# Kernel tuning notes

Hardware: AMD Instinct MI355X
Metric: run time of the kernel (lower is better)

## Reference

```python
import jax, jax.numpy as jnp
import numpy as np

NUM_EMBEDDINGS = 1024
EMBEDDING_DIM = 256
COMMITMENT_COST = 0.25


def setup_inputs() -> dict:
    key = jax.random.key(0)
    k_z, k_e = jax.random.split(key)
    z = jax.random.normal(k_z, (16, EMBEDDING_DIM, 4096), dtype=jnp.float32)
    # nn.Embedding init: uniform(-1/K, 1/K)
    emb = jax.random.uniform(
        k_e, (NUM_EMBEDDINGS, EMBEDDING_DIM), dtype=jnp.float32,
        minval=-1.0 / NUM_EMBEDDINGS, maxval=1.0 / NUM_EMBEDDINGS)
    return {"z": z, "emb": emb}


def reference(z, emb):
    # z: [B, D, T] -> [B, T, D]
    zt = jnp.transpose(z, (0, 2, 1))
    B, T, D = zt.shape
    flat = zt.reshape(-1, D)  # [N, D]
    dists = (jnp.sum(flat * flat, axis=1, keepdims=True)
             + jnp.sum(emb * emb, axis=1)
             - 2.0 * jnp.matmul(flat, emb.T))
    idx = jnp.argmin(dists, axis=1)          # [N]
    quantized = emb[idx].reshape(B, T, D)    # gather + reshape
    e_latent_loss = jnp.mean((jax.lax.stop_gradient(quantized) - zt) ** 2)
    q_latent_loss = jnp.mean((quantized - jax.lax.stop_gradient(zt)) ** 2)
    loss = q_latent_loss + COMMITMENT_COST * e_latent_loss
    # straight-through estimator
    quantized_st = zt + jax.lax.stop_gradient(quantized - zt)
    return jnp.transpose(quantized_st, (0, 2, 1)), loss
```

## Files before the change

kernel.cpp:

```cpp
#include <hip/hip_runtime.h>
#include <stdint.h>

#define B_   16
#define D_   256
#define T_   4096
#define K_   1024
#define N_   (B_ * T_)
#define BM   64

typedef __attribute__((ext_vector_type(4))) float floatx4;
typedef __attribute__((ext_vector_type(2))) float floatx2;
typedef __attribute__((ext_vector_type(2))) long longx2;

__global__ __launch_bounds__(256) void emb_prep(const float* __restrict__ emb,
                                                uint32_t* __restrict__ embf8,
                                                float* __restrict__ esqh,
                                                float* __restrict__ lossp) {
    int w = threadIdx.x >> 6, lane = threadIdx.x & 63;
    int k = blockIdx.x * 4 + w;
    float4 v = ((const float4*)emb)[k * 64 + lane];
    float a0 = v.x * 1024.f, a1 = v.y * 1024.f, a2 = v.z * 1024.f, a3 = v.w * 1024.f;
    int p = __builtin_amdgcn_cvt_pk_fp8_f32(a0, a1, 0, false);
    p = __builtin_amdgcn_cvt_pk_fp8_f32(a2, a3, p, true);
    int kk = lane >> 3, quad = (lane >> 1) & 3;
    int widx = (k >> 4) * 1024 + (kk >> 1) * 256 + (quad * 16 + (k & 15)) * 4
             + (kk & 1) * 2 + (lane & 1);
    embf8[widx] = (uint32_t)p;
    float ss = a0 * a0 + a1 * a1 + a2 * a2 + a3 * a3;
    #pragma unroll
    for (int off = 32; off; off >>= 1) ss += __shfl_xor(ss, off, 64);
    if (lane == 0) esqh[k] = ss * (0.5f / 1024.f);
    if (blockIdx.x == 0 && threadIdx.x == 0) *lossp = 0.f;
}

__global__ __launch_bounds__(256, 3) void vq_main(const float* __restrict__ z,
                                                  const uint32_t* __restrict__ embf8,
                                                  const float* __restrict__ esqh,
                                                  float* __restrict__ out0,
                                                  float* __restrict__ lossp) {
    __shared__ __align__(16) unsigned char xs[BM * 256];
    __shared__ float wvals[4][BM];
    __shared__ int   pidx[BM];
    __shared__ float zred[4];

    int tid  = threadIdx.x;
    int lane = tid & 63, w = tid >> 6;
    int ml   = lane & 15, quad = lane >> 4;
    int blk  = blockIdx.x;
    int b    = blk >> 6;
    int t0   = (blk & 63) * BM;
    const float* zb = z + (size_t)b * (D_ * T_) + t0;

    float zsq = 0.f;
    {
        int t = lane, hf = (t >> 4) & 1;
        #pragma unroll 2
        for (int j = 0; j < 8; ++j) {
            int dgrp = w + 4 * j;
            int d0 = dgrp * 8;
            float f0 = zb[(d0 + 0) * T_ + t];
            float f1 = zb[(d0 + 1) * T_ + t];
            float f2 = zb[(d0 + 2) * T_ + t];
            float f3 = zb[(d0 + 3) * T_ + t];
            float f4 = zb[(d0 + 4) * T_ + t];
            float f5 = zb[(d0 + 5) * T_ + t];
            float f6 = zb[(d0 + 6) * T_ + t];
            float f7 = zb[(d0 + 7) * T_ + t];
            zsq += f0*f0 + f1*f1 + f2*f2 + f3*f3 + f4*f4 + f5*f5 + f6*f6 + f7*f7;
            uint32_t p0 = (uint32_t)__builtin_amdgcn_cvt_pk_fp8_f32(f0, f1, 0, false);
            p0 = (uint32_t)__builtin_amdgcn_cvt_pk_fp8_f32(f2, f3, (int)p0, true);
            uint32_t p1 = (uint32_t)__builtin_amdgcn_cvt_pk_fp8_f32(f4, f5, 0, false);
            p1 = (uint32_t)__builtin_amdgcn_cvt_pk_fp8_f32(f6, f7, (int)p1, true);
            int c = dgrp >> 1, h = dgrp & 1;
            *(uint2*)&xs[t * 256 + ((c ^ (t & 15)) << 4) + ((h ^ hf) << 3)] =
                make_uint2(p0, p1);
        }
    }
    __syncthreads();

    long afr[4][8];
    #pragma unroll
    for (int s = 0; s < 4; ++s) {
        int pnt = s * 16 + ml;
        #pragma unroll
        for (int kk = 0; kk < 8; ++kk) {
            int c = 2 * kk + (quad >> 1), h = quad & 1;
            afr[s][kk] = *(const long*)&xs[pnt * 256 + ((c ^ ml) << 4) + ((h ^ (s & 1)) << 3)];
        }
    }

    float bv[4][4];
    #pragma unroll
    for (int s = 0; s < 4; ++s)
        #pragma unroll
        for (int i = 0; i < 4; ++i) bv[s][i] = 1e30f;

    int ct0 = w * 16;
    const char* ebL = (const char*)embf8 + (size_t)ct0 * 4096 + (size_t)lane * 16;
    const unsigned hi_mask = 0xFFFFFC00u;
    #pragma unroll 2
    for (int j = 0; j < 16; ++j) {
        const char* p = ebL + (size_t)j * 4096;
        longx2 qq[4];
        #pragma unroll
        for (int i = 0; i < 4; ++i)
            qq[i] = *(const longx2*)(p + i * 1024);
        float eh = esqh[(ct0 + j) * 16 + ml];
        floatx4 a0 = {0,0,0,0}, a1 = {0,0,0,0}, a2 = {0,0,0,0}, a3 = {0,0,0,0};
        #pragma unroll
        for (int i = 0; i < 4; ++i) {
            long bf0 = qq[i][0], bf1 = qq[i][1];
            a0 = __builtin_amdgcn_mfma_f32_16x16x32_fp8_fp8(afr[0][2*i],     bf0, a0, 0, 0, 0);
            a1 = __builtin_amdgcn_mfma_f32_16x16x32_fp8_fp8(afr[1][2*i],     bf0, a1, 0, 0, 0);
            a2 = __builtin_amdgcn_mfma_f32_16x16x32_fp8_fp8(afr[2][2*i],     bf0, a2, 0, 0, 0);
            a3 = __builtin_amdgcn_mfma_f32_16x16x32_fp8_fp8(afr[3][2*i],     bf0, a3, 0, 0, 0);
            a0 = __builtin_amdgcn_mfma_f32_16x16x32_fp8_fp8(afr[0][2*i + 1], bf1, a0, 0, 0, 0);
            a1 = __builtin_amdgcn_mfma_f32_16x16x32_fp8_fp8(afr[1][2*i + 1], bf1, a1, 0, 0, 0);
            a2 = __builtin_amdgcn_mfma_f32_16x16x32_fp8_fp8(afr[2][2*i + 1], bf1, a2, 0, 0, 0);
            a3 = __builtin_amdgcn_mfma_f32_16x16x32_fp8_fp8(afr[3][2*i + 1], bf1, a3, 0, 0, 0);
        }
        unsigned cbits = (unsigned)((ct0 + j) * 16 + ml);
        #pragma unroll
        for (int i = 0; i < 4; ++i) {
            float d0 = eh - a0[i];
            bv[0][i] = fminf(bv[0][i], __uint_as_float((__float_as_uint(d0) & hi_mask) | cbits));
            float d1 = eh - a1[i];
            bv[1][i] = fminf(bv[1][i], __uint_as_float((__float_as_uint(d1) & hi_mask) | cbits));
            float d2 = eh - a2[i];
            bv[2][i] = fminf(bv[2][i], __uint_as_float((__float_as_uint(d2) & hi_mask) | cbits));
            float d3 = eh - a3[i];
            bv[3][i] = fminf(bv[3][i], __uint_as_float((__float_as_uint(d3) & hi_mask) | cbits));
        }
    }

    #pragma unroll
    for (int s = 0; s < 4; ++s)
        #pragma unroll
        for (int i = 0; i < 4; ++i) {
            float v = bv[s][i];
            #pragma unroll
            for (int off = 1; off < 16; off <<= 1)
                v = fminf(v, __shfl_xor(v, off, 64));
            if (ml == 0) wvals[w][s * 16 + quad * 4 + i] = v;
        }
    #pragma unroll
    for (int off = 32; off; off >>= 1) zsq += __shfl_xor(zsq, off, 64);
    if (lane == 0) zred[w] = zsq;
    __syncthreads();

    if (tid < 64) {
        int t = tid;
        float wv = fminf(fminf(wvals[0][t], wvals[1][t]),
                         fminf(wvals[2][t], wvals[3][t]));
        pidx[t] = (int)(__float_as_uint(wv) & 1023u);
        float lsum = wv;
        #pragma unroll
        for (int off = 32; off; off >>= 1) lsum += __shfl_xor(lsum, off, 64);
        if (t == 0) {
            float tot = zred[0] + zred[1] + zred[2] + zred[3] + lsum * (2.0f / 1024.f);
            atomicAdd(lossp, tot * (1.25f / 16777216.0f));
        }
    }
    __syncthreads();

    #pragma unroll
    for (int m = 0; m < 4; ++m) {
        int t = (tid >> 4) + 16 * m;
        int g = tid & 15;
        int code = pidx[t];
        const char* src = (const char*)embf8 + (size_t)(code >> 4) * 4096
                        + (g >> 2) * 1024 + ((g & 3) * 16 + (code & 15)) * 16;
        uint4 v = *(const uint4*)src;
        *(uint4*)&xs[t * 256 + ((g ^ (t & 15)) << 4)] = v;
    }
    __syncthreads();

    float* ob = out0 + (size_t)b * (D_ * T_) + t0;
    {
        int t = lane;
        #pragma unroll
        for (int jj = 0; jj < 4; ++jj) {
            int g = w + 4 * jj;
            uint4 v = *(const uint4*)&xs[t * 256 + ((g ^ (t & 15)) << 4)];
            uint32_t wd[4] = {v.x, v.y, v.z, v.w};
            #pragma unroll
            for (int u = 0; u < 4; ++u) {
                int kk = (g >> 2) * 2 + (u >> 1);
                int d0 = kk * 32 + (g & 3) * 8 + (u & 1) * 4;
                floatx2 lo = __builtin_amdgcn_cvt_pk_f32_fp8((int)wd[u], false);
                floatx2 hi = __builtin_amdgcn_cvt_pk_f32_fp8((int)wd[u], true);
                ob[(d0 + 0) * T_ + t] = lo[0] * (1.f / 1024.f);
                ob[(d0 + 1) * T_ + t] = lo[1] * (1.f / 1024.f);
                ob[(d0 + 2) * T_ + t] = hi[0] * (1.f / 1024.f);
                ob[(d0 + 3) * T_ + t] = hi[1] * (1.f / 1024.f);
            }
        }
    }
}

extern "C" void kernel_launch(void* const* d_in, const int* in_sizes, int n_in,
                              void* d_out, int out_size, void* d_ws, size_t ws_size,
                              hipStream_t stream) {
    (void)in_sizes; (void)n_in; (void)out_size; (void)ws_size;
    const float* z   = (const float*)d_in[0];
    const float* emb = (const float*)d_in[1];

    uint32_t* embf8 = (uint32_t*)d_ws;
    float*    esqh  = (float*)((char*)d_ws + (size_t)K_ * D_);

    float* out0  = (float*)d_out;
    float* lossp = out0 + (size_t)N_ * D_;

    emb_prep<<<K_ / 4, 256, 0, stream>>>(emb, embf8, esqh, lossp);
    vq_main<<<N_ / BM, 256, 0, stream>>>(z, embf8, esqh, out0, lossp);
}
```

Before: 146.1 us.

## Halve point tile to 32 and split codebook across 8 waves per block

Reduces the points per block from 64 to 32 and uses 512 threads. Four waves cover the codebook quarters for each 16-point set, and each wave holds one set of A fragments and one accumulator. The goal is higher occupancy and fewer registers per wave. The cost is four times more codebook fragment loads per point and shorter contiguous z reads and output writes.

```diff
diff --git a/kernel.cpp b/kernel.cpp
--- a/kernel.cpp
+++ b/kernel.cpp
@@ -6,7 +6,7 @@
 #define T_   4096
 #define K_   1024
 #define N_   (B_ * T_)
-#define BM   64
+#define BM   32
 
 typedef __attribute__((ext_vector_type(4))) float floatx4;
 typedef __attribute__((ext_vector_type(2))) float floatx2;
@@ -33,30 +33,31 @@
     if (blockIdx.x == 0 && threadIdx.x == 0) *lossp = 0.f;
 }
 
-__global__ __launch_bounds__(256, 3) void vq_main(const float* __restrict__ z,
+__global__ __launch_bounds__(512, 8) void vq_main(const float* __restrict__ z,
                                                   const uint32_t* __restrict__ embf8,
                                                   const float* __restrict__ esqh,
                                                   float* __restrict__ out0,
                                                   float* __restrict__ lossp) {
     __shared__ __align__(16) unsigned char xs[BM * 256];
-    __shared__ float wvals[4][BM];
+    __shared__ float wvals[8][16];
     __shared__ int   pidx[BM];
-    __shared__ float zred[4];
+    __shared__ float zred[8];
 
     int tid  = threadIdx.x;
     int lane = tid & 63, w = tid >> 6;
     int ml   = lane & 15, quad = lane >> 4;
     int blk  = blockIdx.x;
-    int b    = blk >> 6;
-    int t0   = (blk & 63) * BM;
+    int b    = blk >> 7;
+    int t0   = (blk & 127) * BM;
     const float* zb = z + (size_t)b * (D_ * T_) + t0;
 
     float zsq = 0.f;
     {
-        int t = lane, hf = (t >> 4) & 1;
-        #pragma unroll 2
-        for (int j = 0; j < 8; ++j) {
-            int dgrp = w + 4 * j;
+        int t = tid & 31, sl = tid >> 5;
+        int hf = (t >> 4) & 1;
+        #pragma unroll
+        for (int j = 0; j < 2; ++j) {
+            int dgrp = sl + 16 * j;
             int d0 = dgrp * 8;
             float f0 = zb[(d0 + 0) * T_ + t];
             float f1 = zb[(d0 + 1) * T_ + t];
@@ -78,94 +79,79 @@
     }
     __syncthreads();
 
-    long afr[4][8];
-    #pragma unroll
-    for (int s = 0; s < 4; ++s) {
-        int pnt = s * 16 + ml;
+    int set = w >> 2;
+    long afr[8];
+    {
+        int pnt = set * 16 + ml;
         #pragma unroll
         for (int kk = 0; kk < 8; ++kk) {
             int c = 2 * kk + (quad >> 1), h = quad & 1;
-            afr[s][kk] = *(const long*)&xs[pnt * 256 + ((c ^ ml) << 4) + ((h ^ (s & 1)) << 3)];
+            afr[kk] = *(const long*)&xs[pnt * 256 + ((c ^ ml) << 4) + ((h ^ (set & 1)) << 3)];
         }
     }
 
-    float bv[4][4];
+    float bv[4];
     #pragma unroll
-    for (int s = 0; s < 4; ++s)
-        #pragma unroll
-        for (int i = 0; i < 4; ++i) bv[s][i] = 1e30f;
+    for (int i = 0; i < 4; ++i) bv[i] = 1e30f;
 
-    int ct0 = w * 16;
+    int ct0 = (w & 3) * 16;
     const char* ebL = (const char*)embf8 + (size_t)ct0 * 4096 + (size_t)lane * 16;
+    const float* ehp = esqh + ct0 * 16 + ml;
     const unsigned hi_mask = 0xFFFFFC00u;
-    #pragma unroll 2
+    #pragma unroll 1
     for (int j = 0; j < 16; ++j) {
         const char* p = ebL + (size_t)j * 4096;
         longx2 qq[4];
         #pragma unroll
         for (int i = 0; i < 4; ++i)
             qq[i] = *(const longx2*)(p + i * 1024);
-        float eh = esqh[(ct0 + j) * 16 + ml];
-        floatx4 a0 = {0,0,0,0}, a1 = {0,0,0,0}, a2 = {0,0,0,0}, a3 = {0,0,0,0};
+        float eh = ehp[j * 16];
+        floatx4 a0 = {0.f, 0.f, 0.f, 0.f};
         #pragma unroll
         for (int i = 0; i < 4; ++i) {
-            long bf0 = qq[i][0], bf1 = qq[i][1];
-            a0 = __builtin_amdgcn_mfma_f32_16x16x32_fp8_fp8(afr[0][2*i],     bf0, a0, 0, 0, 0);
-            a1 = __builtin_amdgcn_mfma_f32_16x16x32_fp8_fp8(afr[1][2*i],     bf0, a1, 0, 0, 0);
-            a2 = __builtin_amdgcn_mfma_f32_16x16x32_fp8_fp8(afr[2][2*i],     bf0, a2, 0, 0, 0);
-            a3 = __builtin_amdgcn_mfma_f32_16x16x32_fp8_fp8(afr[3][2*i],     bf0, a3, 0, 0, 0);
-            a0 = __builtin_amdgcn_mfma_f32_16x16x32_fp8_fp8(afr[0][2*i + 1], bf1, a0, 0, 0, 0);
-            a1 = __builtin_amdgcn_mfma_f32_16x16x32_fp8_fp8(afr[1][2*i + 1], bf1, a1, 0, 0, 0);
-            a2 = __builtin_amdgcn_mfma_f32_16x16x32_fp8_fp8(afr[2][2*i + 1], bf1, a2, 0, 0, 0);
-            a3 = __builtin_amdgcn_mfma_f32_16x16x32_fp8_fp8(afr[3][2*i + 1], bf1, a3, 0, 0, 0);
+            a0 = __builtin_amdgcn_mfma_f32_16x16x32_fp8_fp8(afr[2*i],     qq[i][0], a0, 0, 0, 0);
+            a0 = __builtin_amdgcn_mfma_f32_16x16x32_fp8_fp8(afr[2*i + 1], qq[i][1], a0, 0, 0, 0);
         }
         unsigned cbits = (unsigned)((ct0 + j) * 16 + ml);
         #pragma unroll
         for (int i = 0; i < 4; ++i) {
-            float d0 = eh - a0[i];
-            bv[0][i] = fminf(bv[0][i], __uint_as_float((__float_as_uint(d0) & hi_mask) | cbits));
-            float d1 = eh - a1[i];
-            bv[1][i] = fminf(bv[1][i], __uint_as_float((__float_as_uint(d1) & hi_mask) | cbits));
-            float d2 = eh - a2[i];
-            bv[2][i] = fminf(bv[2][i], __uint_as_float((__float_as_uint(d2) & hi_mask) | cbits));
-            float d3 = eh - a3[i];
-            bv[3][i] = fminf(bv[3][i], __uint_as_float((__float_as_uint(d3) & hi_mask) | cbits));
+            float dv = eh - a0[i];
+            bv[i] = fminf(bv[i], __uint_as_float((__float_as_uint(dv) & hi_mask) | cbits));
         }
     }
 
     #pragma unroll
-    for (int s = 0; s < 4; ++s)
+    for (int i = 0; i < 4; ++i) {
+        float v = bv[i];
         #pragma unroll
-        for (int i = 0; i < 4; ++i) {
-            float v = bv[s][i];
-            #pragma unroll
-            for (int off = 1; off < 16; off <<= 1)
-                v = fminf(v, __shfl_xor(v, off, 64));
-            if (ml == 0) wvals[w][s * 16 + quad * 4 + i] = v;
-        }
+        for (int off = 1; off < 16; off <<= 1)
+            v = fminf(v, __shfl_xor(v, off, 64));
+        if (ml == 0) wvals[w][quad * 4 + i] = v;
+    }
     #pragma unroll
     for (int off = 32; off; off >>= 1) zsq += __shfl_xor(zsq, off, 64);
     if (lane == 0) zred[w] = zsq;
     __syncthreads();
 
-    if (tid < 64) {
-        int t = tid;
-        float wv = fminf(fminf(wvals[0][t], wvals[1][t]),
-                         fminf(wvals[2][t], wvals[3][t]));
+    if (tid < 32) {
+        int t = tid, qb = (t >> 4) * 4, pis = t & 15;
+        float wv = fminf(fminf(wvals[qb][pis], wvals[qb + 1][pis]),
+                         fminf(wvals[qb + 2][pis], wvals[qb + 3][pis]));
         pidx[t] = (int)(__float_as_uint(wv) & 1023u);
         float lsum = wv;
         #pragma unroll
-        for (int off = 32; off; off >>= 1) lsum += __shfl_xor(lsum, off, 64);
+        for (int off = 16; off; off >>= 1) lsum += __shfl_xor(lsum, off, 64);
         if (t == 0) {
-            float tot = zred[0] + zred[1] + zred[2] + zred[3] + lsum * (2.0f / 1024.f);
+            float tot = zred[0] + zred[1] + zred[2] + zred[3]
+                      + zred[4] + zred[5] + zred[6] + zred[7]
+                      + lsum * (2.0f / 1024.f);
             atomicAdd(lossp, tot * (1.25f / 16777216.0f));
         }
     }
     __syncthreads();
 
-    #pragma unroll
-    for (int m = 0; m < 4; ++m) {
-        int t = (tid >> 4) + 16 * m;
+    {
+        int t = tid >> 4;
         int g = tid & 15;
         int code = pidx[t];
         const char* src = (const char*)embf8 + (size_t)(code >> 4) * 4096
@@ -177,23 +163,19 @@
 
     float* ob = out0 + (size_t)b * (D_ * T_) + t0;
     {
-        int t = lane;
+        int t = tid & 31, g = tid >> 5;
+        uint4 v = *(const uint4*)&xs[t * 256 + ((g ^ (t & 15)) << 4)];
+        uint32_t wd[4] = {v.x, v.y, v.z, v.w};
         #pragma unroll
-        for (int jj = 0; jj < 4; ++jj) {
-            int g = w + 4 * jj;
-            uint4 v = *(const uint4*)&xs[t * 256 + ((g ^ (t & 15)) << 4)];
-            uint32_t wd[4] = {v.x, v.y, v.z, v.w};
-            #pragma unroll
-            for (int u = 0; u < 4; ++u) {
-                int kk = (g >> 2) * 2 + (u >> 1);
-                int d0 = kk * 32 + (g & 3) * 8 + (u & 1) * 4;
-                floatx2 lo = __builtin_amdgcn_cvt_pk_f32_fp8((int)wd[u], false);
-                floatx2 hi = __builtin_amdgcn_cvt_pk_f32_fp8((int)wd[u], true);
-                ob[(d0 + 0) * T_ + t] = lo[0] * (1.f / 1024.f);
-                ob[(d0 + 1) * T_ + t] = lo[1] * (1.f / 1024.f);
-                ob[(d0 + 2) * T_ + t] = hi[0] * (1.f / 1024.f);
-                ob[(d0 + 3) * T_ + t] = hi[1] * (1.f / 1024.f);
-            }
+        for (int u = 0; u < 4; ++u) {
+            int kk = (g >> 2) * 2 + (u >> 1);
+            int d0 = kk * 32 + (g & 3) * 8 + (u & 1) * 4;
+            floatx2 lo = __builtin_amdgcn_cvt_pk_f32_fp8((int)wd[u], false);
+            floatx2 hi = __builtin_amdgcn_cvt_pk_f32_fp8((int)wd[u], true);
+            ob[(d0 + 0) * T_ + t] = lo[0] * (1.f / 1024.f);
+            ob[(d0 + 1) * T_ + t] = lo[1] * (1.f / 1024.f);
+            ob[(d0 + 2) * T_ + t] = hi[0] * (1.f / 1024.f);
+            ob[(d0 + 3) * T_ + t] = hi[1] * (1.f / 1024.f);
         }
     }
 }
@@ -212,5 +194,5 @@
     float* lossp = out0 + (size_t)N_ * D_;
 
     emb_prep<<<K_ / 4, 256, 0, stream>>>(emb, embf8, esqh, lossp);
-    vq_main<<<N_ / BM, 256, 0, stream>>>(z, embf8, esqh, out0, lossp);
+    vq_main<<<N_ / BM, 512, 0, stream>>>(z, embf8, esqh, out0, lossp);
 }
```

Result: slower. 159.8 us (+9.4%).
